# Optimization experiments

Hardware: AMD Instinct MI355X
Metric: run time of the kernel (lower is better)

Reference implementation:

```python
import jax, jax.numpy as jnp
import numpy as np

S, N, D, F, E = 2048, 8, 1024, 4096, 8
STD = 0.02


def setup_inputs() -> dict:
    key = jax.random.key(0)
    ks = jax.random.split(key, 5)
    x = jax.random.normal(ks[0], (S, N, D), dtype=jnp.float32)
    Wg = jax.random.normal(ks[1], (E, D), dtype=jnp.float32) * STD
    W1 = jax.random.normal(ks[2], (E, F, D), dtype=jnp.float32) * STD
    b1 = jnp.zeros((E, F), dtype=jnp.float32)
    W2 = jax.random.normal(ks[3], (E, D, F), dtype=jnp.float32) * STD
    b2 = jnp.zeros((E, D), dtype=jnp.float32)
    return {"x": x, "Wg": Wg, "W1": W1, "b1": b1, "W2": W2, "b2": b2}


def reference(x, Wg, W1, b1, W2, b2):
    # Gate (eval mode: no gating noise). scores: [S, N, E]
    scores = jnp.einsum('snd,ed->sne', x, Wg)
    prob = jax.nn.softmax(scores, axis=-1)
    top1_idx = jnp.argmax(prob, axis=-1)                                   # [S, N] int
    top1_prob = jnp.take_along_axis(prob, top1_idx[..., None], axis=-1)[..., 0]  # [S, N]

    y = jnp.zeros_like(x)
    n_experts = Wg.shape[0]
    for e in range(n_experts):  # small fixed loop over experts
        h = jax.nn.gelu(jnp.einsum('snd,fd->snf', x, W1[e]) + b1[e], approximate=False)
        ye = jnp.einsum('snf,df->snd', h, W2[e]) + b2[e]
        mask = (top1_idx == e)[..., None]                                  # [S, N, 1]
        y = y + jnp.where(mask, ye * top1_prob[..., None], 0.0)
    return y
```

## Files before the change

### kernel.cpp

```cpp
#include <hip/hip_runtime.h>

#define S_TOK 16384
#define D_DIM 1024
#define F_DIM 4096
#define E_NUM 8

#define BM 256
#define BN 256
#define BK 64
#define MT_MAX 72

typedef short bf16x8 __attribute__((ext_vector_type(8)));
typedef float f32x4 __attribute__((ext_vector_type(4)));
typedef unsigned short ushort_t;

static __device__ __forceinline__ unsigned short f32_bf16(float f) {
  unsigned u = __float_as_uint(f);
  return (unsigned short)((u + 0x7FFFu + ((u >> 16) & 1u)) >> 16);
}

static __device__ __forceinline__ unsigned int pack_bf16x2(float a, float b) {
  unsigned ua = __float_as_uint(a);
  unsigned ub = __float_as_uint(b);
  unsigned lo = (ua + 0x7FFFu + ((ua >> 16) & 1u)) >> 16;
  unsigned hi = (ub + 0x7FFFu + ((ub >> 16) & 1u)) & 0xFFFF0000u;
  return lo | hi;
}

static __device__ __forceinline__ uint2 cvt_f4_bf4(const float4 v) {
  uint2 r;
  r.x = pack_bf16x2(v.x, v.y);
  r.y = pack_bf16x2(v.z, v.w);
  return r;
}

static __device__ __forceinline__ void load_lds16(const void* g, void* l) {
  __builtin_amdgcn_global_load_lds(g, l, 16, 0, 0);
}

__global__ void zero_counts_kernel(int* counts) {
  if (threadIdx.x < E_NUM) counts[threadIdx.x] = 0;
}

__global__ void cast2_kernel(const float* __restrict__ w1, ushort_t* __restrict__ o1,
                             const float* __restrict__ w2, ushort_t* __restrict__ o2) {
  const int half = 16384;
  const float* src = (blockIdx.x < half) ? w1 : w2;
  ushort_t* dst = (blockIdx.x < half) ? o1 : o2;
  const int b = (blockIdx.x < half) ? blockIdx.x : (blockIdx.x - half);
  const size_t base = ((size_t)b * blockDim.x + threadIdx.x) * 8;
  const float4 v0 = *(const float4*)(src + base);
  const float4 v1 = *(const float4*)(src + base + 4);
  const uint2 a = cvt_f4_bf4(v0), c = cvt_f4_bf4(v1);
  uint4 w; w.x = a.x; w.y = a.y; w.z = c.x; w.w = c.y;
  *(uint4*)(dst + base) = w;
}

__global__ void gate_kernel(const float* __restrict__ x,
                            const float* __restrict__ Wg,
                            ushort_t* __restrict__ xbf,
                            float* __restrict__ prob,
                            int* __restrict__ counts,
                            int* __restrict__ tok_list) {
  const int wv = threadIdx.x >> 6;
  const int lane = threadIdx.x & 63;
  const int t = blockIdx.x * 4 + wv;
  const float* xr = x + (size_t)t * D_DIM;
  ushort_t* xb = xbf + (size_t)t * D_DIM;

  float acc[E_NUM];
#pragma unroll
  for (int e = 0; e < E_NUM; ++e) acc[e] = 0.0f;

#pragma unroll
  for (int i = 0; i < 4; ++i) {
    const int k = i * 256 + lane * 4;
    const float4 v = *(const float4*)(xr + k);
    *(uint2*)(xb + k) = cvt_f4_bf4(v);
#pragma unroll
    for (int e = 0; e < E_NUM; ++e) {
      const float4 w = *(const float4*)(Wg + e * D_DIM + k);
      acc[e] += v.x * w.x + v.y * w.y + v.z * w.z + v.w * w.w;
    }
  }
#pragma unroll
  for (int e = 0; e < E_NUM; ++e) {
#pragma unroll
    for (int off = 32; off > 0; off >>= 1)
      acc[e] += __shfl_xor(acc[e], off, 64);
  }
  if (lane == 0) {
    float m = acc[0]; int bi = 0;
#pragma unroll
    for (int e = 1; e < E_NUM; ++e) {
      if (acc[e] > m) { m = acc[e]; bi = e; }
    }
    float s = 0.0f;
#pragma unroll
    for (int e = 0; e < E_NUM; ++e) s += expf(acc[e] - m);
    prob[t] = 1.0f / s;
    int p = atomicAdd(&counts[bi], 1);
    tok_list[bi * S_TOK + p] = t;
  }
}

__global__ void plan_kernel(const int* __restrict__ counts, int* __restrict__ plan) {
  if (threadIdx.x == 0) {
    int t = 0;
    for (int e = 0; e < E_NUM; ++e) {
      const int nt = (counts[e] + BM - 1) / BM;
      for (int i = 0; i < nt; ++i) {
        plan[1 + t] = e;
        plan[1 + MT_MAX + t] = i * BM;
        ++t;
      }
    }
    plan[0] = t;
  }
}

template <int KDIM, int NDIM, int EPI>
__launch_bounds__(512, 2)
__global__ void ffn_kernel(const ushort_t* __restrict__ A,
                           const ushort_t* __restrict__ B,
                           const float* __restrict__ bias,
                           const float* __restrict__ prob,
                           const int* __restrict__ counts,
                           const int* __restrict__ tok_list,
                           const int* __restrict__ plan,
                           ushort_t* __restrict__ Hout,
                           float* __restrict__ out) {
  constexpr int NT = NDIM / BN;
  constexpr int NWG = NT * MT_MAX;
  constexpr int NK = KDIM / BK;
  const int ntiles = plan[0];
  const int wg = (blockIdx.x & 7) * (NWG >> 3) + (blockIdx.x >> 3);
  const int tile = wg / NT;
  if (tile >= ntiles) return;
  const int n0 = (wg % NT) * BN;
  const int e = plan[1 + tile];
  const int m0 = plan[1 + MT_MAX + tile];
  const int cnt = counts[e];

  __shared__ ushort_t Lds[2][2][BM * BK];

  const int tid = threadIdx.x;
  const int lane = tid & 63;
  const int wid = tid >> 6;
  const int wr2 = wid >> 2;
  const int wc4 = wid & 3;
  const int l15 = lane & 15;
  const int l4  = lane >> 4;

  const int srow = tid >> 3;
  const int sslot = ((tid & 7) ^ (srow & 7)) * 8;
  const int dstoff = wid * 512;

  const size_t ebase = (size_t)e * S_TOK;
  const ushort_t* aS[4];
  const ushort_t* bS[4];
  const ushort_t* Bebase = B + (size_t)e * NDIM * KDIM;
#pragma unroll
  for (int i = 0; i < 4; ++i) {
    const int ra = m0 + i * 64 + srow;
    const int tok = (ra < cnt) ? tok_list[ebase + ra] : 0;
    aS[i] = A + (size_t)tok * KDIM + sslot;
    bS[i] = Bebase + (size_t)(n0 + i * 64 + srow) * KDIM + sslot;
  }

  int oA[8][2], oB[4][2];
#pragma unroll
  for (int m = 0; m < 8; ++m) {
    const int r = wr2 * 128 + m * 16 + l15;
#pragma unroll
    for (int kk = 0; kk < 2; ++kk)
      oA[m][kk] = r * BK + (((kk * 4 + l4) ^ (r & 7)) * 8);
  }
#pragma unroll
  for (int n = 0; n < 4; ++n) {
    const int r = wc4 * 64 + n * 16 + l15;
#pragma unroll
    for (int kk = 0; kk < 2; ++kk)
      oB[n][kk] = r * BK + (((kk * 4 + l4) ^ (r & 7)) * 8);
  }

  f32x4 acc[8][4];
#pragma unroll
  for (int i = 0; i < 8; ++i)
#pragma unroll
    for (int j = 0; j < 4; ++j)
      acc[i][j] = (f32x4){0.f, 0.f, 0.f, 0.f};

#pragma unroll
  for (int i = 0; i < 4; ++i) {
    load_lds16(aS[i], &Lds[0][0][i * 4096 + dstoff]);
    load_lds16(bS[i], &Lds[0][1][i * 4096 + dstoff]);
  }
  __syncthreads();

  int cb = 0;
  for (int t = 0; t < NK; ++t) {
    if (t + 1 < NK) {
      const int k0 = (t + 1) * BK;
      const int nb = cb ^ 1;
#pragma unroll
      for (int i = 0; i < 4; ++i) {
        load_lds16(aS[i] + k0, &Lds[nb][0][i * 4096 + dstoff]);
        load_lds16(bS[i] + k0, &Lds[nb][1][i * 4096 + dstoff]);
      }
    }

#pragma unroll
    for (int kk = 0; kk < 2; ++kk) {
      bf16x8 a[8], b[4];
#pragma unroll
      for (int m = 0; m < 8; ++m) a[m] = *(const bf16x8*)&Lds[cb][0][oA[m][kk]];
#pragma unroll
      for (int n = 0; n < 4; ++n) b[n] = *(const bf16x8*)&Lds[cb][1][oB[n][kk]];
#pragma unroll
      for (int m = 0; m < 8; ++m)
#pragma unroll
        for (int n = 0; n < 4; ++n)
          acc[m][n] = __builtin_amdgcn_mfma_f32_16x16x32_bf16(a[m], b[n], acc[m][n], 0, 0, 0);
    }

    __syncthreads();
    cb ^= 1;
  }

  const float* be = bias + (size_t)e * NDIM;
#pragma unroll
  for (int m = 0; m < 8; ++m) {
#pragma unroll
    for (int r = 0; r < 4; ++r) {
      const int slot = m0 + wr2 * 128 + m * 16 + l4 * 4 + r;
      if (slot >= cnt) continue;
      const int tok = tok_list[ebase + slot];
      if (EPI == 0) {
        ushort_t* hrow = Hout + (size_t)tok * NDIM;
#pragma unroll
        for (int n = 0; n < 4; ++n) {
          const int col = n0 + wc4 * 64 + n * 16 + l15;
          float v = acc[m][n][r] + be[col];
          v = 0.5f * v * (1.0f + erff(v * 0.70710678118654752f));
          hrow[col] = f32_bf16(v);
        }
      } else {
        const float p = prob[tok];
        float* orow = out + (size_t)tok * NDIM;
#pragma unroll
        for (int n = 0; n < 4; ++n) {
          const int col = n0 + wc4 * 64 + n * 16 + l15;
          orow[col] = (acc[m][n][r] + be[col]) * p;
        }
      }
    }
  }
}

extern "C" void kernel_launch(void* const* d_in, const int* in_sizes, int n_in,
                              void* d_out, int out_size, void* d_ws, size_t ws_size,
                              hipStream_t stream) {
  const float* x  = (const float*)d_in[0];
  const float* Wg = (const float*)d_in[1];
  const float* W1 = (const float*)d_in[2];
  const float* b1 = (const float*)d_in[3];
  const float* W2 = (const float*)d_in[4];
  const float* b2 = (const float*)d_in[5];
  float* out = (float*)d_out;

  const size_t MB = 1ull << 20;
  char* ws = (char*)d_ws;
  int* counts      = (int*)(ws);
  int* plan        = (int*)(ws + 4096);
  float* prob      = (float*)(ws + 64 * 1024);
  int* tok_list    = (int*)(ws + 128 * 1024);
  ushort_t* xbf    = (ushort_t*)(ws + 1 * MB);
  ushort_t* W1bf   = (ushort_t*)(ws + 33 * MB);
  ushort_t* W2bf   = (ushort_t*)(ws + 97 * MB);
  ushort_t* H      = (ushort_t*)(ws + 161 * MB);

  zero_counts_kernel<<<1, 64, 0, stream>>>(counts);
  gate_kernel<<<S_TOK / 4, 256, 0, stream>>>(x, Wg, xbf, prob, counts, tok_list);
  plan_kernel<<<1, 64, 0, stream>>>(counts, plan);

  cast2_kernel<<<32768, 256, 0, stream>>>(W1, W1bf, W2, W2bf);

  ffn_kernel<D_DIM, F_DIM, 0><<<(F_DIM / BN) * MT_MAX, 512, 0, stream>>>(
      xbf, W1bf, b1, nullptr, counts, tok_list, plan, H, nullptr);

  ffn_kernel<F_DIM, D_DIM, 1><<<(D_DIM / BN) * MT_MAX, 512, 0, stream>>>(
      H, W2bf, b2, prob, counts, tok_list, plan, nullptr, out);
}
```

Measured before the change: 822.0 us.

## Deepen LDS prefetch to two stages and compact XCD tile mapping to live tiles

Restructures the main K loop so two tiles are in flight. The loop waits on vmcnt(8) plus a raw barrier, and the load for tile t+2 is issued into the buffer just consumed. This is meant to hide global-to-LDS latency better than the single-ahead prefetch with __syncthreads. The workgroup-to-XCD remap now spreads only the live tiles (ntiles*NT) evenly across the 8 XCDs instead of a fixed MT_MAX grid, so empty workgroups exit early and load balance improves. It relies on a hand-counted vmcnt and issues redundant clamped loads at the tail.

```diff
diff --git a/kernel.cpp b/kernel.cpp
--- a/kernel.cpp
+++ b/kernel.cpp
@@ -131,12 +131,14 @@
                            ushort_t* __restrict__ Hout,
                            float* __restrict__ out) {
   constexpr int NT = NDIM / BN;
-  constexpr int NWG = NT * MT_MAX;
   constexpr int NK = KDIM / BK;
   const int ntiles = plan[0];
-  const int wg = (blockIdx.x & 7) * (NWG >> 3) + (blockIdx.x >> 3);
+  const int live = ntiles * NT;
+  if (blockIdx.x >= live) return;
+  const int q = live >> 3, r = live & 7;
+  const int xcd = blockIdx.x & 7, idx = blockIdx.x >> 3;
+  const int wg = (xcd < r ? xcd * (q + 1) : r * (q + 1) + (xcd - r) * q) + idx;
   const int tile = wg / NT;
-  if (tile >= ntiles) return;
   const int n0 = (wg % NT) * BN;
   const int e = plan[1 + tile];
   const int m0 = plan[1 + MT_MAX + tile];
@@ -171,17 +173,17 @@
   int oA[8][2], oB[4][2];
 #pragma unroll
   for (int m = 0; m < 8; ++m) {
-    const int r = wr2 * 128 + m * 16 + l15;
+    const int rr = wr2 * 128 + m * 16 + l15;
 #pragma unroll
     for (int kk = 0; kk < 2; ++kk)
-      oA[m][kk] = r * BK + (((kk * 4 + l4) ^ (r & 7)) * 8);
+      oA[m][kk] = rr * BK + (((kk * 4 + l4) ^ (rr & 7)) * 8);
   }
 #pragma unroll
   for (int n = 0; n < 4; ++n) {
-    const int r = wc4 * 64 + n * 16 + l15;
+    const int rr = wc4 * 64 + n * 16 + l15;
 #pragma unroll
     for (int kk = 0; kk < 2; ++kk)
-      oB[n][kk] = r * BK + (((kk * 4 + l4) ^ (r & 7)) * 8);
+      oB[n][kk] = rr * BK + (((kk * 4 + l4) ^ (rr & 7)) * 8);
   }
 
   f32x4 acc[8][4];
@@ -196,19 +198,20 @@
     load_lds16(aS[i], &Lds[0][0][i * 4096 + dstoff]);
     load_lds16(bS[i], &Lds[0][1][i * 4096 + dstoff]);
   }
-  __syncthreads();
-
-  int cb = 0;
+  {
+    const int k1 = (NK > 1) ? BK : 0;
+#pragma unroll
+    for (int i = 0; i < 4; ++i) {
+      load_lds16(aS[i] + k1, &Lds[1][0][i * 4096 + dstoff]);
+      load_lds16(bS[i] + k1, &Lds[1][1][i * 4096 + dstoff]);
+    }
+  }
+
   for (int t = 0; t < NK; ++t) {
-    if (t + 1 < NK) {
-      const int k0 = (t + 1) * BK;
-      const int nb = cb ^ 1;
-#pragma unroll
-      for (int i = 0; i < 4; ++i) {
-        load_lds16(aS[i] + k0, &Lds[nb][0][i * 4096 + dstoff]);
-        load_lds16(bS[i] + k0, &Lds[nb][1][i * 4096 + dstoff]);
-      }
-    }
+    const int cb = t & 1;
+    asm volatile("s_waitcnt vmcnt(8)" ::: "memory");
+    __builtin_amdgcn_s_barrier();
+    __builtin_amdgcn_sched_barrier(0);
 
 #pragma unroll
     for (int kk = 0; kk < 2; ++kk) {
@@ -224,16 +227,23 @@
           acc[m][n] = __builtin_amdgcn_mfma_f32_16x16x32_bf16(a[m], b[n], acc[m][n], 0, 0, 0);
     }
 
-    __syncthreads();
-    cb ^= 1;
+    __builtin_amdgcn_sched_barrier(0);
+    __builtin_amdgcn_s_barrier();
+
+    const int k2 = ((t + 2 < NK) ? (t + 2) : (NK - 1)) * BK;
+#pragma unroll
+    for (int i = 0; i < 4; ++i) {
+      load_lds16(aS[i] + k2, &Lds[cb][0][i * 4096 + dstoff]);
+      load_lds16(bS[i] + k2, &Lds[cb][1][i * 4096 + dstoff]);
+    }
   }
 
   const float* be = bias + (size_t)e * NDIM;
 #pragma unroll
   for (int m = 0; m < 8; ++m) {
 #pragma unroll
-    for (int r = 0; r < 4; ++r) {
-      const int slot = m0 + wr2 * 128 + m * 16 + l4 * 4 + r;
+    for (int rr = 0; rr < 4; ++rr) {
+      const int slot = m0 + wr2 * 128 + m * 16 + l4 * 4 + rr;
       if (slot >= cnt) continue;
       const int tok = tok_list[ebase + slot];
       if (EPI == 0) {
@@ -241,7 +251,7 @@
 #pragma unroll
         for (int n = 0; n < 4; ++n) {
           const int col = n0 + wc4 * 64 + n * 16 + l15;
-          float v = acc[m][n][r] + be[col];
+          float v = acc[m][n][rr] + be[col];
           v = 0.5f * v * (1.0f + erff(v * 0.70710678118654752f));
           hrow[col] = f32_bf16(v);
         }
@@ -251,7 +261,7 @@
 #pragma unroll
         for (int n = 0; n < 4; ++n) {
           const int col = n0 + wc4 * 64 + n * 16 + l15;
-          orow[col] = (acc[m][n][r] + be[col]) * p;
+          orow[col] = (acc[m][n][rr] + be[col]) * p;
         }
       }
     }
```

Result: slower. 877.8 us (+6.8%).
